# Kernel tuning notes

Hardware: AMD Instinct MI355X
Metric: run time of the kernel (lower is better)

The kernel has to match this reference:

```python
import jax, jax.numpy as jnp
import numpy as np

EPS = 1e-05  # module eps (both LayerNorm and mask-count denominator)


def setup_inputs() -> dict:
    key = jax.random.key(0)
    ks = jax.random.split(key, 6)
    b, m, n, dm, dh, dp = 1, 256, 384, 256, 32, 128
    x = jax.random.normal(ks[0], (b, m, n, dm), jnp.float32)
    mask = jnp.ones((b, m, n), dtype=bool)
    ln_g = jnp.ones((dm,), jnp.float32)
    ln_b = jnp.zeros((dm,), jnp.float32)
    wl = jax.random.normal(ks[1], (dm, dh), jnp.float32) * 0.02
    bl = jnp.zeros((dh,), jnp.float32)
    wr = jax.random.normal(ks[2], (dm, dh), jnp.float32) * 0.02
    br = jnp.zeros((dh,), jnp.float32)
    wo = jax.random.normal(ks[3], (dh * dh, dp), jnp.float32) * 0.02
    bo = jnp.zeros((dp,), jnp.float32)
    return dict(x=x, mask=mask, ln_g=ln_g, ln_b=ln_b, wl=wl, bl=bl,
                wr=wr, br=br, wo=wo, bo=bo)


def reference(x, mask, ln_g, ln_b, wl, bl, wr, br, wo, bo):
    # x: (b, m, i, dim_msa); mask: (b, m, i)
    mu = jnp.mean(x, axis=-1, keepdims=True)
    var = jnp.var(x, axis=-1, keepdims=True)
    xn = (x - mu) / jnp.sqrt(var + EPS) * ln_g + ln_b

    mf = mask.astype(x.dtype)  # (b, m, i)
    # mask_i * mask_j on the outer product == masking left and right separately
    left = (xn @ wl + bl) * mf[..., None]   # (b, m, i, dh)
    right = (xn @ wr + br) * mf[..., None]  # (b, m, j, dh)

    # sum over MSA depth m without materializing the (b,m,i,j,c,d) tensor
    outer = jnp.einsum('bmic,bmjd->bijcd', left, right)  # (b, i, j, dh, dh)
    b_, n_ = outer.shape[0], outer.shape[1]
    out = outer.reshape(b_, n_, n_, -1) @ wo + bo  # (b, i, j, dim_pairwise)

    # normalize by pairwise mask count (matches masked branch of the module)
    count = jnp.einsum('bmi,bmj->bij', mf, mf)[..., None]  # (b, i, j, 1)
    return out / (count + EPS)
```

## Files before the change

### kernel.cpp

```cpp
#include <hip/hip_runtime.h>
#include <hip/hip_bf16.h>

#define EPS 1e-5f
#define MM 256
#define NN 384
#define DM 256
#define DH 32
#define DP 128
#define NIC (NN*DH)

typedef __attribute__((ext_vector_type(8))) short short8;
typedef __attribute__((ext_vector_type(4))) float floatx4;

__device__ __forceinline__ void load16_to_lds(const void* gptr, void* lptr) {
    __builtin_amdgcn_global_load_lds(
        (const __attribute__((address_space(1))) void*)gptr,
        (__attribute__((address_space(3))) void*)lptr,
        16, 0, 0);
}

__device__ __forceinline__ unsigned short f2bf_bits(float f) {
    __hip_bfloat16 h = __float2bfloat16(f);
    union { __hip_bfloat16 h; unsigned short u; } cvt;
    cvt.h = h;
    return cvt.u;
}

__global__ __launch_bounds__(256) void k0a_woT(
    const float* __restrict__ wo, unsigned short* __restrict__ woT2)
{
    __shared__ float ts[64*129];
    const int s  = blockIdx.x >> 2;
    const int dg = blockIdx.x & 3;
    const int t  = threadIdx.x;
    #pragma unroll
    for (int g = 0; g < 32; g++) {
        int idx = g*256 + t;
        int row = idx >> 7, p = idx & 127;
        int ci = row >> 3, di = row & 7;
        int cd = (s*8 + ci)*32 + dg*8 + di;
        ts[row*129 + p] = wo[(size_t)cd*DP + p];
    }
    __syncthreads();
    int p = t >> 1, half = t & 1;
    #pragma unroll
    for (int dq = 0; dq < 4; dq++) {
        int di = half*4 + dq;
        #pragma unroll
        for (int cq = 0; cq < 2; cq++) {
            ushort4 u;
            u.x = f2bf_bits(ts[((cq*4+0)*8 + di)*129 + p]);
            u.y = f2bf_bits(ts[((cq*4+1)*8 + di)*129 + p]);
            u.z = f2bf_bits(ts[((cq*4+2)*8 + di)*129 + p]);
            u.w = f2bf_bits(ts[((cq*4+3)*8 + di)*129 + p]);
            *(ushort4*)&woT2[(size_t)p*1024 + s*256 + dg*64 + di*8 + cq*4] = u;
        }
    }
}

__global__ __launch_bounds__(256) void k0b_w(
    const float* __restrict__ wl, const float* __restrict__ bl,
    const float* __restrict__ wr, const float* __restrict__ br,
    unsigned short* __restrict__ WbT, float* __restrict__ bias)
{
    const int t = threadIdx.x;
    for (int g = 0; g < 64; g++) {
        int idx = g*256 + t;
        int c = idx >> 8, k = idx & 255;
        float v = (c < DH) ? wl[k*DH + c] : wr[k*DH + (c - DH)];
        WbT[c*256 + k] = f2bf_bits(v);
    }
    if (t < 64) bias[t] = (t < DH) ? bl[t] : br[t - DH];
}

__global__ __launch_bounds__(256) void k2a_pack(
    const int* __restrict__ mask, unsigned int* __restrict__ pack)
{
    int id = blockIdx.x*256 + threadIdx.x;
    if (id >= NN*8) return;
    int i = id >> 3, tw = id & 7;
    unsigned int wbits = 0;
    #pragma unroll
    for (int b = 0; b < 32; b++)
        wbits |= (mask[(tw*32 + b)*NN + i] != 0 ? 1u : 0u) << b;
    pack[id] = wbits;
}

__global__ __launch_bounds__(256) void k2_count(
    const unsigned int* __restrict__ pack, float* __restrict__ cinv)
{
    int id = blockIdx.x * 256 + threadIdx.x;
    int i = id / NN, j = id % NN;
    int s = 0;
    #pragma unroll
    for (int tw = 0; tw < 8; tw++)
        s += __popc(pack[i*8 + tw] & pack[j*8 + tw]);
    cinv[id] = 1.0f / ((float)s + EPS);
}

__global__ __launch_bounds__(256) void k1_lnproj(
    const float* __restrict__ x, const int* __restrict__ mask,
    const float* __restrict__ ln_g, const float* __restrict__ ln_b,
    const unsigned short* __restrict__ WbTg, const float* __restrict__ bias,
    unsigned short* __restrict__ Lb, unsigned short* __restrict__ Rb)
{
    __shared__ unsigned short xns[64*264];
    __shared__ float mfs[64];

    const int i  = blockIdx.x;
    const int mc = blockIdx.y;
    const int t = threadIdx.x;
    const int l = t & 63, w = t >> 6;
    const int lc = l & 15, quad = l >> 4;

    float4 g4 = *(const float4*)&ln_g[l*4];
    float4 b4 = *(const float4*)&ln_b[l*4];

    for (int rr = 0; rr < 16; rr++) {
        int mlocal = w*16 + rr;
        int m = mc*64 + mlocal;
        size_t grow = (size_t)m*NN + i;
        float4 v = *(const float4*)&x[grow*DM + l*4];
        float s  = v.x + v.y + v.z + v.w;
        float s2 = v.x*v.x + v.y*v.y + v.z*v.z + v.w*v.w;
        #pragma unroll
        for (int off = 1; off < 64; off <<= 1) {
            s  += __shfl_xor(s,  off, 64);
            s2 += __shfl_xor(s2, off, 64);
        }
        float mu   = s * (1.0f/DM);
        float var  = s2 * (1.0f/DM) - mu*mu;
        float rstd = rsqrtf(var + EPS);
        ushort4 u;
        u.x = f2bf_bits((v.x - mu)*rstd*g4.x + b4.x);
        u.y = f2bf_bits((v.y - mu)*rstd*g4.y + b4.y);
        u.z = f2bf_bits((v.z - mu)*rstd*g4.z + b4.z);
        u.w = f2bf_bits((v.w - mu)*rstd*g4.w + b4.w);
        *(ushort4*)&xns[mlocal*264 + l*4] = u;
        if (l == 0) mfs[mlocal] = (mask[grow] != 0) ? 1.0f : 0.0f;
    }
    __syncthreads();

    floatx4 acc[4];
    #pragma unroll
    for (int nt = 0; nt < 4; nt++) acc[nt] = (floatx4){0.f,0.f,0.f,0.f};
    #pragma unroll
    for (int ks = 0; ks < 8; ks++) {
        short8 af = *(const short8*)&xns[(w*16 + lc)*264 + ks*32 + quad*8];
        #pragma unroll
        for (int nt = 0; nt < 4; nt++) {
            short8 bf = *(const short8*)&WbTg[(nt*16 + lc)*256 + ks*32 + quad*8];
            acc[nt] = __builtin_amdgcn_mfma_f32_16x16x32_bf16(af, bf, acc[nt], 0, 0, 0);
        }
    }
    __syncthreads();

    unsigned short* tr = xns;
    #pragma unroll
    for (int nt = 0; nt < 4; nt++) {
        int c = nt*16 + lc;
        float bv = bias[c];
        #pragma unroll
        for (int rg = 0; rg < 4; rg++) {
            int mlocal = w*16 + quad*4 + rg;
            tr[c*72 + mlocal] = f2bf_bits((acc[nt][rg] + bv) * mfs[mlocal]);
        }
    }
    __syncthreads();

    {
        int c = t >> 2, seg = t & 3;
        unsigned short* dst = (c < DH)
            ? &Lb[((size_t)(i*DH + c))*MM + mc*64 + seg*16]
            : &Rb[((size_t)(i*DH + (c - DH)))*MM + mc*64 + seg*16];
        #pragma unroll
        for (int q = 0; q < 4; q++)
            *(ushort4*)&dst[q*4] = *(ushort4*)&tr[c*72 + seg*16 + q*4];
    }
}

__global__ __launch_bounds__(512, 2) void k3f_gemm(
    const unsigned short* __restrict__ Lb,
    const unsigned short* __restrict__ Rb,
    const unsigned short* __restrict__ woT2,
    const float* __restrict__ bo, const float* __restrict__ cinv,
    float* __restrict__ out)
{
    __shared__ short smem[32768];
    const int t = threadIdx.x;
    const int l = t & 63, w = t >> 6;
    const int wx = w & 3, wy = w >> 2;
    const int lc = l & 15, quad = l >> 4;

    int bid = blockIdx.x;
    int swz = (bid & 7) * 288 + (bid >> 3);
    int bx = swz % 48, by = swz / 48;

    const size_t arow0 = (size_t)bx * 256;
    const size_t brow0 = (size_t)by * 256;

    const int pos0 = t, pos1 = 512 + t;
    const int line0 = pos0 >> 3, c0 = (pos0 & 7) ^ (line0 & 7);
    const int r0 = line0*2 + (c0 >> 2), k00 = (c0 & 3) * 8;
    const int line1 = pos1 >> 3, c1 = (pos1 & 7) ^ (line1 & 7);
    const int r1 = line1*2 + (c1 >> 2), k01 = (c1 & 3) * 8;

    const unsigned short* srcA0 = Lb + (arow0 + r0)*MM + k00;
    const unsigned short* srcA1 = Lb + (arow0 + r1)*MM + k01;
    const unsigned short* srcB0 = Rb + (brow0 + r0)*MM + k00;
    const unsigned short* srcB1 = Rb + (brow0 + r1)*MM + k01;

    floatx4 acc[8][4];
    #pragma unroll
    for (int a = 0; a < 8; a++)
        #pragma unroll
        for (int b = 0; b < 4; b++) acc[a][b] = (floatx4){0.f,0.f,0.f,0.f};

#define STAGE(bsel, step) do {                                           \
        char* sb = (char*)smem + (bsel)*32768;                           \
        load16_to_lds(srcA0 + (step)*32, sb + pos0*16);                  \
        load16_to_lds(srcA1 + (step)*32, sb + pos1*16);                  \
        load16_to_lds(srcB0 + (step)*32, sb + 16384 + pos0*16);          \
        load16_to_lds(srcB1 + (step)*32, sb + 16384 + pos1*16);          \
    } while (0)

    STAGE(0, 0);
    STAGE(1, 1);
    #pragma unroll
    for (int tstep = 0; tstep < 8; tstep++) {
        if (tstep < 7) asm volatile("s_waitcnt vmcnt(4)" ::: "memory");
        else           asm volatile("s_waitcnt vmcnt(0)" ::: "memory");
        __builtin_amdgcn_s_barrier();
        __builtin_amdgcn_sched_barrier(0);
        const char* Ab = (const char*)smem + (tstep & 1)*32768;
        const char* Bb = Ab + 16384;
        short8 bfr[4];
        #pragma unroll
        for (int nt = 0; nt < 4; nt++) {
            int r = wx*64 + nt*16 + lc;
            int li = r >> 1, cc = ((r & 1)*4 + quad) ^ (li & 7);
            bfr[nt] = *(const short8*)(Bb + li*128 + cc*16);
        }
        __builtin_amdgcn_s_setprio(1);
        #pragma unroll
        for (int mt = 0; mt < 8; mt++) {
            int r = wy*128 + mt*16 + lc;
            int li = r >> 1, cc = ((r & 1)*4 + quad) ^ (li & 7);
            short8 af = *(const short8*)(Ab + li*128 + cc*16);
            #pragma unroll
            for (int nt = 0; nt < 4; nt++)
                acc[mt][nt] = __builtin_amdgcn_mfma_f32_16x16x32_bf16(
                    af, bfr[nt], acc[mt][nt], 0, 0, 0);
        }
        __builtin_amdgcn_s_setprio(0);
        __builtin_amdgcn_s_barrier();
        __builtin_amdgcn_sched_barrier(0);
        if (tstep + 2 < 8) STAGE(tstep & 1, tstep + 2);
    }
#undef STAGE

    short* gp = smem;
    const int prow = w*16 + lc;
    floatx4 acc2[4];
    #pragma unroll
    for (int a = 0; a < 4; a++) acc2[a] = (floatx4){0.f,0.f,0.f,0.f};

    #pragma unroll
    for (int s = 0; s < 4; s++) {
        short8 b2r[8];
        #pragma unroll
        for (int ks = 0; ks < 8; ks++)
            b2r[ks] = *(const short8*)&woT2[(size_t)prow*1024 + s*256 + ks*32 + quad*8];

        if ((quad >> 1) == (s & 1)) {
            #pragma unroll
            for (int mmi = 0; mmi < 4; mmi++) {
                const int mt = (s >> 1) + mmi*2;
                #pragma unroll
                for (int nt = 0; nt < 4; nt++) {
                    int pair = (wy*4 + (mt >> 1))*8 + (wx*2 + (nt >> 1));
                    int d = (nt & 1)*16 + lc;
                    int kk = d*8 + (quad & 1)*4;
                    ushort4 u;
                    u.x = f2bf_bits(acc[mt][nt][0]);
                    u.y = f2bf_bits(acc[mt][nt][1]);
                    u.z = f2bf_bits(acc[mt][nt][2]);
                    u.w = f2bf_bits(acc[mt][nt][3]);
                    *(ushort4*)&gp[pair*264 + kk] = u;
                }
            }
        }
        __syncthreads();

        __builtin_amdgcn_s_setprio(1);
        #pragma unroll
        for (int ks = 0; ks < 8; ks++) {
            #pragma unroll
            for (int mt2 = 0; mt2 < 4; mt2++) {
                short8 a2 = *(const short8*)&gp[(mt2*16 + lc)*264 + ks*32 + quad*8];
                acc2[mt2] = __builtin_amdgcn_mfma_f32_16x16x32_bf16(
                    a2, b2r[ks], acc2[mt2], 0, 0, 0);
            }
        }
        __builtin_amdgcn_s_setprio(0);
        __syncthreads();
    }

    const float bv = bo[prow];
    #pragma unroll
    for (int mt2 = 0; mt2 < 4; mt2++) {
        #pragma unroll
        for (int rg = 0; rg < 4; rg++) {
            int pair = mt2*16 + quad*4 + rg;
            int i = bx*8 + (pair >> 3);
            int j = by*8 + (pair & 7);
            out[((size_t)(i*NN + j))*DP + prow] =
                (acc2[mt2][rg] + bv) * cinv[i*NN + j];
        }
    }
}

extern "C" void kernel_launch(void* const* d_in, const int* in_sizes, int n_in,
                              void* d_out, int out_size, void* d_ws, size_t ws_size,
                              hipStream_t stream)
{
    const float* x    = (const float*)d_in[0];
    const int*   mask = (const int*)d_in[1];
    const float* ln_g = (const float*)d_in[2];
    const float* ln_b = (const float*)d_in[3];
    const float* wl   = (const float*)d_in[4];
    const float* bl   = (const float*)d_in[5];
    const float* wr   = (const float*)d_in[6];
    const float* br   = (const float*)d_in[7];
    const float* wo   = (const float*)d_in[8];
    const float* bo   = (const float*)d_in[9];
    float* out = (float*)d_out;

    char* ws = (char*)d_ws;
    size_t off = 0;
    unsigned short* Lb   = (unsigned short*)(ws + off); off += (size_t)NIC*MM*2;
    unsigned short* Rb   = (unsigned short*)(ws + off); off += (size_t)NIC*MM*2;
    unsigned short* woT2 = (unsigned short*)(ws + off); off += (size_t)DP*1024*2;
    unsigned short* WbTg = (unsigned short*)(ws + off); off += (size_t)64*256*2;
    float*          bias = (float*)(ws + off);          off += 64*4;
    float*          cinv = (float*)(ws + off);          off += (size_t)NN*NN*4;
    unsigned int*   pack = (unsigned int*)Lb;

    k0a_woT<<<16, 256, 0, stream>>>(wo, woT2);
    k0b_w<<<1, 256, 0, stream>>>(wl, bl, wr, br, WbTg, bias);
    k2a_pack<<<12, 256, 0, stream>>>(mask, pack);
    k2_count<<<(NN*NN)/256, 256, 0, stream>>>(pack, cinv);
    k1_lnproj<<<dim3(NN, MM/64), 256, 0, stream>>>(x, mask, ln_g, ln_b, WbTg, bias, Lb, Rb);
    k3f_gemm<<<2304, 512, 0, stream>>>(Lb, Rb, woT2, bo, cinv, out);
}
```

Measured before the change: 401.1 us.

## Parallelize weight prep, batch LayerNorm loads, and remap GEMM block swizzle

The weight transpose kernel now runs on 64 blocks instead of a single block looping 64 times, and the mask pack kernel uses a simpler 8x384 grid. The LayerNorm stage issues all 16 float4 loads per thread up front, with 4 rows handled per wave in parallel, so the reduction needs only a 16-lane shuffle. It also gets a 4-waves-per-SIMD launch bound. The main GEMM changes its block-to-tile mapping so each XCD owns a contiguous band of B tiles, aiming for better L2 reuse. The extra registers held for the prefetched values may limit occupancy.

New measurement: 356.2 us. 1.13x faster.

```diff
diff --git a/kernel.cpp b/kernel.cpp
--- a/kernel.cpp
+++ b/kernel.cpp
@@ -63,27 +63,21 @@
     const float* __restrict__ wr, const float* __restrict__ br,
     unsigned short* __restrict__ WbT, float* __restrict__ bias)
 {
-    const int t = threadIdx.x;
-    for (int g = 0; g < 64; g++) {
-        int idx = g*256 + t;
-        int c = idx >> 8, k = idx & 255;
-        float v = (c < DH) ? wl[k*DH + c] : wr[k*DH + (c - DH)];
-        WbT[c*256 + k] = f2bf_bits(v);
-    }
-    if (t < 64) bias[t] = (t < DH) ? bl[t] : br[t - DH];
-}
-
-__global__ __launch_bounds__(256) void k2a_pack(
+    const int c = blockIdx.x, k = threadIdx.x;
+    float v = (c < DH) ? wl[k*DH + c] : wr[k*DH + (c - DH)];
+    WbT[c*256 + k] = f2bf_bits(v);
+    if (c == 0 && k < 64) bias[k] = (k < DH) ? bl[k] : br[k - DH];
+}
+
+__global__ __launch_bounds__(384) void k2a_pack(
     const int* __restrict__ mask, unsigned int* __restrict__ pack)
 {
-    int id = blockIdx.x*256 + threadIdx.x;
-    if (id >= NN*8) return;
-    int i = id >> 3, tw = id & 7;
+    int tw = blockIdx.x, i = threadIdx.x;
     unsigned int wbits = 0;
     #pragma unroll
     for (int b = 0; b < 32; b++)
         wbits |= (mask[(tw*32 + b)*NN + i] != 0 ? 1u : 0u) << b;
-    pack[id] = wbits;
+    pack[i*8 + tw] = wbits;
 }
 
 __global__ __launch_bounds__(256) void k2_count(
@@ -98,7 +92,7 @@
     cinv[id] = 1.0f / ((float)s + EPS);
 }
 
-__global__ __launch_bounds__(256) void k1_lnproj(
+__global__ __launch_bounds__(256, 4) void k1_lnproj(
     const float* __restrict__ x, const int* __restrict__ mask,
     const float* __restrict__ ln_g, const float* __restrict__ ln_b,
     const unsigned short* __restrict__ WbTg, const float* __restrict__ bias,
@@ -112,32 +106,56 @@
     const int t = threadIdx.x;
     const int l = t & 63, w = t >> 6;
     const int lc = l & 15, quad = l >> 4;
-
-    float4 g4 = *(const float4*)&ln_g[l*4];
-    float4 b4 = *(const float4*)&ln_b[l*4];
-
-    for (int rr = 0; rr < 16; rr++) {
-        int mlocal = w*16 + rr;
+    const int sub = l >> 4, lc4 = l & 15;
+
+    float4 gk[4], bk[4];
+    #pragma unroll
+    for (int g = 0; g < 4; g++) {
+        gk[g] = *(const float4*)&ln_g[g*64 + lc4*4];
+        bk[g] = *(const float4*)&ln_b[g*64 + lc4*4];
+    }
+
+    float4 v[4][4];
+    #pragma unroll
+    for (int rr = 0; rr < 4; rr++) {
+        int mlocal = w*16 + rr*4 + sub;
         int m = mc*64 + mlocal;
-        size_t grow = (size_t)m*NN + i;
-        float4 v = *(const float4*)&x[grow*DM + l*4];
-        float s  = v.x + v.y + v.z + v.w;
-        float s2 = v.x*v.x + v.y*v.y + v.z*v.z + v.w*v.w;
-        #pragma unroll
-        for (int off = 1; off < 64; off <<= 1) {
+        const float4* xr = (const float4*)&x[((size_t)m*NN + i)*DM];
+        #pragma unroll
+        for (int g = 0; g < 4; g++)
+            v[rr][g] = xr[g*16 + lc4];
+    }
+
+    #pragma unroll
+    for (int rr = 0; rr < 4; rr++) {
+        int mlocal = w*16 + rr*4 + sub;
+        int m = mc*64 + mlocal;
+        float s = 0.f, s2 = 0.f;
+        #pragma unroll
+        for (int g = 0; g < 4; g++) {
+            float4 vg = v[rr][g];
+            s  += vg.x + vg.y + vg.z + vg.w;
+            s2 += vg.x*vg.x + vg.y*vg.y + vg.z*vg.z + vg.w*vg.w;
+        }
+        #pragma unroll
+        for (int off = 1; off < 16; off <<= 1) {
             s  += __shfl_xor(s,  off, 64);
             s2 += __shfl_xor(s2, off, 64);
         }
         float mu   = s * (1.0f/DM);
         float var  = s2 * (1.0f/DM) - mu*mu;
         float rstd = rsqrtf(var + EPS);
-        ushort4 u;
-        u.x = f2bf_bits((v.x - mu)*rstd*g4.x + b4.x);
-        u.y = f2bf_bits((v.y - mu)*rstd*g4.y + b4.y);
-        u.z = f2bf_bits((v.z - mu)*rstd*g4.z + b4.z);
-        u.w = f2bf_bits((v.w - mu)*rstd*g4.w + b4.w);
-        *(ushort4*)&xns[mlocal*264 + l*4] = u;
-        if (l == 0) mfs[mlocal] = (mask[grow] != 0) ? 1.0f : 0.0f;
+        #pragma unroll
+        for (int g = 0; g < 4; g++) {
+            float4 vg = v[rr][g];
+            ushort4 u;
+            u.x = f2bf_bits((vg.x - mu)*rstd*gk[g].x + bk[g].x);
+            u.y = f2bf_bits((vg.y - mu)*rstd*gk[g].y + bk[g].y);
+            u.z = f2bf_bits((vg.z - mu)*rstd*gk[g].z + bk[g].z);
+            u.w = f2bf_bits((vg.w - mu)*rstd*gk[g].w + bk[g].w);
+            *(ushort4*)&xns[mlocal*264 + g*64 + lc4*4] = u;
+        }
+        if (lc4 == 0) mfs[mlocal] = (mask[(size_t)m*NN + i] != 0) ? 1.0f : 0.0f;
     }
     __syncthreads();
 
@@ -193,8 +211,10 @@
     const int lc = l & 15, quad = l >> 4;
 
     int bid = blockIdx.x;
-    int swz = (bid & 7) * 288 + (bid >> 3);
-    int bx = swz % 48, by = swz / 48;
+    int xcd = bid & 7;
+    int local = bid >> 3;
+    int bx = local / 6;
+    int by = xcd * 6 + (local % 6);
 
     const size_t arow0 = (size_t)bx * 256;
     const size_t brow0 = (size_t)by * 256;
@@ -347,8 +367,8 @@
     unsigned int*   pack = (unsigned int*)Lb;
 
     k0a_woT<<<16, 256, 0, stream>>>(wo, woT2);
-    k0b_w<<<1, 256, 0, stream>>>(wl, bl, wr, br, WbTg, bias);
-    k2a_pack<<<12, 256, 0, stream>>>(mask, pack);
+    k0b_w<<<64, 256, 0, stream>>>(wl, bl, wr, br, WbTg, bias);
+    k2a_pack<<<8, 384, 0, stream>>>(mask, pack);
     k2_count<<<(NN*NN)/256, 256, 0, stream>>>(pack, cinv);
     k1_lnproj<<<dim3(NN, MM/64), 256, 0, stream>>>(x, mask, ln_g, ln_b, WbTg, bias, Lb, Rb);
     k3f_gemm<<<2304, 512, 0, stream>>>(Lb, Rb, woT2, bo, cinv, out);
```
